# Optimization experiments

Measured on AMD Instinct MI355X. Metric: run time of the kernel, lower is better.

Reference implementation:

```python
import jax, jax.numpy as jnp
import numpy as np

E = 1024
H = 16
DH = E // H
S = 2048
K_NEIGHBOURS = 64
MASKING_VALUE = -1e10  # fp32 branch of the original module


def setup_inputs() -> dict:
    key = jax.random.key(0)
    ks = jax.random.split(key, 5)
    return {
        "x": jax.random.normal(ks[0], (S, E), dtype=jnp.float32),
        "W_qkv": jax.random.normal(ks[1], (3 * E, E), dtype=jnp.float32) * (E ** -0.5),
        "b_qkv": jax.random.normal(ks[2], (3 * E,), dtype=jnp.float32) * 0.02,
        "W_out": jax.random.normal(ks[3], (E, E), dtype=jnp.float32) * (E ** -0.5),
        "b_out": jax.random.normal(ks[4], (E,), dtype=jnp.float32) * 0.02,
    }


def _heads(t):
    # 's (h d) -> h s d'
    return t.reshape(S, H, DH).transpose(1, 0, 2)


def reference(x, W_qkv, b_qkv, W_out, b_out):
    scale = DH ** -0.5
    qkv = x @ W_qkv.T + b_qkv                      # [S, 3E]
    q, k, v = jnp.split(qkv, 3, axis=-1)
    q, k, v = _heads(q), _heads(k), _heads(v)      # [H, S, DH]
    scores = jnp.einsum('hsd,htd->hst', q, k) * scale  # [H, S, S]
    # banded mask: keep |i-j| <= K_NEIGHBOURS
    idx = jnp.arange(S)
    band = jnp.abs(idx[:, None] - idx[None, :]) <= K_NEIGHBOURS  # [S, S]
    scores = jnp.where(band[None, :, :], scores, MASKING_VALUE)
    attn = jax.nn.softmax(scores, axis=-1)
    out = jnp.einsum('hst,htd->hsd', attn, v)      # [H, S, DH]
    out = out.transpose(1, 0, 2).reshape(S, E)      # 'h s d -> s (h d)'
    out = out @ W_out.T + b_out
    return (out, scores)
```

## Files before the change

kernel.cpp:

```cpp
#include <hip/hip_runtime.h>

typedef unsigned short u16;
typedef __attribute__((ext_vector_type(8))) short short8;
typedef __attribute__((ext_vector_type(4))) short short4v;
typedef __attribute__((ext_vector_type(4))) float f32x4;

#define S_LEN 2048
#define EMB   1024
#define NH    16
#define DHD   64
#define NEGM  (-1e10f)

__device__ __forceinline__ u16 f2bf(float f) {
  unsigned u = __float_as_uint(f);
  u += 0x7fffu + ((u >> 16) & 1u);
  return (u16)(u >> 16);
}

__device__ __forceinline__ void async16(const u16* g, u16* l) {
  __builtin_amdgcn_global_load_lds(
      (const __attribute__((address_space(1))) unsigned int*)g,
      (__attribute__((address_space(3))) unsigned int*)l, 16, 0, 0);
}

__global__ __launch_bounds__(256) void cast_bf16_kernel(
    const float* __restrict__ in, u16* __restrict__ out, int n) {
  int t = (blockIdx.x * 256 + threadIdx.x) * 8;
  if (t >= n) return;
  float4 a = *(const float4*)(in + t);
  float4 b = *(const float4*)(in + t + 4);
  u16 r[8];
  r[0] = f2bf(a.x); r[1] = f2bf(a.y); r[2] = f2bf(a.z); r[3] = f2bf(a.w);
  r[4] = f2bf(b.x); r[5] = f2bf(b.y); r[6] = f2bf(b.z); r[7] = f2bf(b.w);
  *(short8*)(out + t) = *(short8*)r;
}

__global__ __launch_bounds__(256, 2) void gemm_bt(
    const u16* __restrict__ A, const u16* __restrict__ B,
    const float* __restrict__ bias, void* __restrict__ Cout,
    int M, int N, int K, int out_bf16) {
  __shared__ u16 As[128 * 64];
  __shared__ u16 Bs[128 * 64];
  const int tid = threadIdx.x;
  const int lane = tid & 63, wave = tid >> 6;
  const int lr = lane & 15, lg = lane >> 4;
  const int m0 = blockIdx.y * 128, n0 = blockIdx.x * 128;
  const int wm = (wave >> 1) * 64, wn = (wave & 1) * 64;

  f32x4 acc[4][4];
#pragma unroll
  for (int i = 0; i < 4; ++i)
#pragma unroll
    for (int j = 0; j < 4; ++j) acc[i][j] = (f32x4){0.f, 0.f, 0.f, 0.f};

  for (int kt = 0; kt < K; kt += 64) {
#pragma unroll
    for (int it = 0; it < 4; ++it) {
      int f = it * 256 + tid;
      int row = f >> 3, ch = f & 7;
      int sch = ch ^ (row & 7);
      const u16* ga = A + (size_t)(m0 + row) * K + kt + sch * 8;
      const u16* gb = B + (size_t)(n0 + row) * K + kt + sch * 8;
      u16* la = &As[(it * 256 + wave * 64) * 8];
      u16* lb = &Bs[(it * 256 + wave * 64) * 8];
      async16(ga, la);
      async16(gb, lb);
    }
    __syncthreads();
#pragma unroll
    for (int kk = 0; kk < 2; ++kk) {
      short8 af[4], bfr[4];
#pragma unroll
      for (int t = 0; t < 4; ++t) {
        int ra = wm + t * 16 + lr;
        int ca = kk * 4 + lg;
        af[t] = *(const short8*)&As[ra * 64 + ((ca ^ (ra & 7)) << 3)];
        int rb = wn + t * 16 + lr;
        bfr[t] = *(const short8*)&Bs[rb * 64 + ((ca ^ (rb & 7)) << 3)];
      }
#pragma unroll
      for (int i = 0; i < 4; ++i)
#pragma unroll
        for (int j = 0; j < 4; ++j)
          acc[i][j] = __builtin_amdgcn_mfma_f32_16x16x32_bf16(af[i], bfr[j],
                                                              acc[i][j], 0, 0, 0);
    }
    __syncthreads();
  }
#pragma unroll
  for (int j = 0; j < 4; ++j) {
    int col = n0 + wn + j * 16 + lr;
    float bv = bias[col];
#pragma unroll
    for (int i = 0; i < 4; ++i) {
#pragma unroll
      for (int r = 0; r < 4; ++r) {
        int row = m0 + wm + i * 16 + lg * 4 + r;
        float v = acc[i][j][r] + bv;
        if (out_bf16)
          ((u16*)Cout)[(size_t)row * N + col] = f2bf(v);
        else
          ((float*)Cout)[(size_t)row * N + col] = v;
      }
    }
  }
}

__global__ __launch_bounds__(256, 2) void attn_kernel(
    const u16* __restrict__ qkv,
    float* __restrict__ scores,
    u16* __restrict__ ctx) {
  const int h = blockIdx.y;
  const int i0 = blockIdx.x * 64;
  const int j0 = i0 - 64;
  const int tid = threadIdx.x;
  const int lane = tid & 63, wave = tid >> 6;
  const int lr = lane & 15, lg = lane >> 4;

  __shared__ u16 Kl[192 * 72];
  __shared__ u16 Vt[64 * 200];
  __shared__ u16 Pl[64 * 200];

#pragma unroll
  for (int it = 0; it < 6; ++it) {
    int f = it * 256 + tid;
    int jr = f >> 3, ch = f & 7;
    int j = j0 + jr;
    short8 kv = {0, 0, 0, 0, 0, 0, 0, 0};
    short8 vv = {0, 0, 0, 0, 0, 0, 0, 0};
    if ((unsigned)j < 2048u) {
      kv = *(const short8*)(qkv + (size_t)j * 3072 + 1024 + h * 64 + ch * 8);
      vv = *(const short8*)(qkv + (size_t)j * 3072 + 2048 + h * 64 + ch * 8);
    }
    *(short4v*)&Kl[jr * 72 + ch * 8] = __builtin_shufflevector(kv, kv, 0, 1, 2, 3);
    *(short4v*)&Kl[jr * 72 + ch * 8 + 4] = __builtin_shufflevector(kv, kv, 4, 5, 6, 7);
#pragma unroll
    for (int e = 0; e < 8; ++e) Vt[(ch * 8 + e) * 200 + jr] = (u16)(short)vv[e];
  }
  __syncthreads();

  short8 qf[2];
#pragma unroll
  for (int kk = 0; kk < 2; ++kk)
    qf[kk] = *(const short8*)(qkv + (size_t)(i0 + wave * 16 + lr) * 3072 +
                              h * 64 + kk * 32 + lg * 8);

  f32x4 sa[12];
#pragma unroll
  for (int n = 0; n < 12; ++n) sa[n] = (f32x4){0.f, 0.f, 0.f, 0.f};
#pragma unroll
  for (int kk = 0; kk < 2; ++kk) {
    short8 a = qf[kk];
#pragma unroll
    for (int nt = 0; nt < 12; ++nt) {
      int jr = nt * 16 + lr;
      int d = kk * 32 + lg * 8;
      short4v lo = *(const short4v*)&Kl[jr * 72 + d];
      short4v hi = *(const short4v*)&Kl[jr * 72 + d + 4];
      short8 b = __builtin_shufflevector(lo, hi, 0, 1, 2, 3, 4, 5, 6, 7);
      sa[nt] = __builtin_amdgcn_mfma_f32_16x16x32_bf16(a, b, sa[nt], 0, 0, 0);
    }
  }

  const float scale = 0.125f;
#pragma unroll
  for (int nt = 0; nt < 12; ++nt) {
    int j = j0 + nt * 16 + lr;
#pragma unroll
    for (int r = 0; r < 4; ++r) {
      int i = i0 + wave * 16 + lg * 4 + r;
      bool inb = (j >= 0) && (j < 2048) && (j >= i - 64) && (j <= i + 64);
      sa[nt][r] = inb ? sa[nt][r] * scale : NEGM;
    }
  }

  float* srow_base = scores + (size_t)h * 2048 * 2048;

#pragma unroll
  for (int r = 0; r < 4; ++r) {
    int i = i0 + wave * 16 + lg * 4 + r;
    float* rowp = srow_base + (size_t)i * 2048;
#pragma unroll
    for (int nt = 0; nt < 12; ++nt) {
      int j = j0 + nt * 16 + lr;
      if (j >= 0 && j < 2048 && j >= i - 64 && j <= i + 64) rowp[j] = sa[nt][r];
    }
  }

#pragma unroll
  for (int r = 0; r < 4; ++r) {
    float m = sa[0][r];
#pragma unroll
    for (int nt = 1; nt < 12; ++nt) m = fmaxf(m, sa[nt][r]);
#pragma unroll
    for (int off = 1; off < 16; off <<= 1) m = fmaxf(m, __shfl_xor(m, off));
    float p[12], s = 0.f;
#pragma unroll
    for (int nt = 0; nt < 12; ++nt) {
      p[nt] = __expf(sa[nt][r] - m);
      s += p[nt];
    }
#pragma unroll
    for (int off = 1; off < 16; off <<= 1) s += __shfl_xor(s, off);
    float inv = 1.f / s;
    int row = wave * 16 + lg * 4 + r;
#pragma unroll
    for (int nt = 0; nt < 12; ++nt)
      Pl[row * 200 + nt * 16 + lr] = f2bf(p[nt] * inv);
  }
  __syncthreads();

  f32x4 ca[4];
#pragma unroll
  for (int d = 0; d < 4; ++d) ca[d] = (f32x4){0.f, 0.f, 0.f, 0.f};
#pragma unroll
  for (int kk = 0; kk < 6; ++kk) {
    short8 a = *(const short8*)&Pl[(wave * 16 + lr) * 200 + kk * 32 + lg * 8];
#pragma unroll
    for (int dt = 0; dt < 4; ++dt) {
      short8 b = *(const short8*)&Vt[(dt * 16 + lr) * 200 + kk * 32 + lg * 8];
      ca[dt] = __builtin_amdgcn_mfma_f32_16x16x32_bf16(a, b, ca[dt], 0, 0, 0);
    }
  }
#pragma unroll
  for (int dt = 0; dt < 4; ++dt)
#pragma unroll
    for (int r = 0; r < 4; ++r) {
      int i = i0 + wave * 16 + lg * 4 + r;
      int d = h * 64 + dt * 16 + lr;
      ctx[(size_t)i * 1024 + d] = f2bf(ca[dt][r]);
    }

  float4 negv = {NEGM, NEGM, NEGM, NEGM};
  for (int r = 0; r < 64; ++r) {
    int i = i0 + r;
    int li = (i - 64 > 0) ? (i - 64) : 0;
    int ri = ((i + 64 < 2047) ? (i + 64) : 2047) + 1;
    float* rowp = srow_base + (size_t)i * 2048;
    for (int c = tid; c < 512; c += 256) {
      int j4 = c << 2;
      if (j4 + 4 <= li || j4 >= ri) {
        *(float4*)(rowp + j4) = negv;
      } else if (j4 < li || j4 + 4 > ri) {
#pragma unroll
        for (int e = 0; e < 4; ++e) {
          int jj = j4 + e;
          if (jj < li || jj >= ri) rowp[jj] = NEGM;
        }
      }
    }
  }
}

extern "C" void kernel_launch(void* const* d_in, const int* in_sizes, int n_in,
                              void* d_out, int out_size, void* d_ws, size_t ws_size,
                              hipStream_t stream) {
  const float* x    = (const float*)d_in[0];
  const float* Wqkv = (const float*)d_in[1];
  const float* bqkv = (const float*)d_in[2];
  const float* Wout = (const float*)d_in[3];
  const float* bout = (const float*)d_in[4];

  float* out    = (float*)d_out;
  float* scores = out + (size_t)S_LEN * EMB;

  char* ws = (char*)d_ws;
  u16* x_bf    = (u16*)(ws);
  u16* wqkv_bf = (u16*)(ws + (4u << 20));
  u16* wout_bf = (u16*)(ws + (10u << 20));
  u16* qkv_bf  = (u16*)(ws + (12u << 20));
  u16* ctx_bf  = (u16*)(ws + (24u << 20));

  const int n1 = S_LEN * EMB;
  const int n2 = 3 * EMB * EMB;
  const int n3 = EMB * EMB;
  cast_bf16_kernel<<<n1 / 8 / 256, 256, 0, stream>>>(x, x_bf, n1);
  cast_bf16_kernel<<<n2 / 8 / 256, 256, 0, stream>>>(Wqkv, wqkv_bf, n2);
  cast_bf16_kernel<<<n3 / 8 / 256, 256, 0, stream>>>(Wout, wout_bf, n3);

  gemm_bt<<<dim3(3 * EMB / 128, S_LEN / 128), 256, 0, stream>>>(
      x_bf, wqkv_bf, bqkv, qkv_bf, S_LEN, 3 * EMB, EMB, 1);

  attn_kernel<<<dim3(S_LEN / 64, NH), 256, 0, stream>>>(qkv_bf, scores, ctx_bf);

  gemm_bt<<<dim3(EMB / 128, S_LEN / 128), 256, 0, stream>>>(
      ctx_bf, wout_bf, bout, out, S_LEN, EMB, EMB, 0);
}
```

Baseline: 381.1 us.

## Overlap masked-score fill with QKV GEMM and merge the cast launches

The full -1e10 fill of the scores tensor moves out of the attention kernel into extra blocks of the QKV GEMM launch, using nontemporal stores so the bandwidth-bound fill runs alongside compute-bound GEMM work. The attention kernel then writes its whole 192-wide window (masked values included) with nontemporal stores, overwriting the prefilled values. The three cast kernels are merged into one launch. The output projection switches to 64x128 tiles to give 256 blocks instead of 128. This relies on the fill finishing before attention writes, which stream ordering guarantees. The fill blocks compete with GEMM blocks for CUs.

```diff
diff --git a/kernel.cpp b/kernel.cpp
--- a/kernel.cpp
+++ b/kernel.cpp
@@ -8,7 +8,6 @@
 #define S_LEN 2048
 #define EMB   1024
 #define NH    16
-#define DHD   64
 #define NEGM  (-1e10f)
 
 __device__ __forceinline__ u16 f2bf(float f) {
@@ -23,81 +22,111 @@
       (__attribute__((address_space(3))) unsigned int*)l, 16, 0, 0);
 }
 
-__global__ __launch_bounds__(256) void cast_bf16_kernel(
-    const float* __restrict__ in, u16* __restrict__ out, int n) {
+__global__ __launch_bounds__(256) void cast3_kernel(
+    const float* __restrict__ a, u16* __restrict__ oa, int na,
+    const float* __restrict__ b, u16* __restrict__ ob, int nb,
+    const float* __restrict__ c, u16* __restrict__ oc, int nc) {
   int t = (blockIdx.x * 256 + threadIdx.x) * 8;
-  if (t >= n) return;
-  float4 a = *(const float4*)(in + t);
-  float4 b = *(const float4*)(in + t + 4);
+  const float* in;
+  u16* out;
+  if (t < na) { in = a + t; out = oa + t; }
+  else if (t < na + nb) { in = b + (t - na); out = ob + (t - na); }
+  else if (t < na + nb + nc) { in = c + (t - na - nb); out = oc + (t - na - nb); }
+  else return;
+  f32x4 lo = *(const f32x4*)(in);
+  f32x4 hi = *(const f32x4*)(in + 4);
   u16 r[8];
-  r[0] = f2bf(a.x); r[1] = f2bf(a.y); r[2] = f2bf(a.z); r[3] = f2bf(a.w);
-  r[4] = f2bf(b.x); r[5] = f2bf(b.y); r[6] = f2bf(b.z); r[7] = f2bf(b.w);
-  *(short8*)(out + t) = *(short8*)r;
-}
-
-__global__ __launch_bounds__(256, 2) void gemm_bt(
+  r[0] = f2bf(lo.x); r[1] = f2bf(lo.y); r[2] = f2bf(lo.z); r[3] = f2bf(lo.w);
+  r[4] = f2bf(hi.x); r[5] = f2bf(hi.y); r[6] = f2bf(hi.z); r[7] = f2bf(hi.w);
+  *(short8*)(out) = *(short8*)r;
+}
+
+template <int BM, int BN, int OUT_BF16, int MINW>
+__global__ __launch_bounds__(256, MINW) void gemm_kernel(
     const u16* __restrict__ A, const u16* __restrict__ B,
     const float* __restrict__ bias, void* __restrict__ Cout,
-    int M, int N, int K, int out_bf16) {
-  __shared__ u16 As[128 * 64];
-  __shared__ u16 Bs[128 * 64];
+    int M, int N, int K, int grid_x, int gemm_blocks,
+    float* __restrict__ fill_ptr, long long fill_f4, int fill_blocks) {
+  __shared__ u16 As[BM * 64];
+  __shared__ u16 Bs[BN * 64];
+  const int b = blockIdx.x;
   const int tid = threadIdx.x;
+
+  if (b >= gemm_blocks) {
+    const long long fb = b - gemm_blocks;
+    f32x4 neg = {NEGM, NEGM, NEGM, NEGM};
+    f32x4* p = (f32x4*)fill_ptr;
+    const long long stride = (long long)fill_blocks * 256;
+    for (long long idx = fb * 256 + tid; idx < fill_f4; idx += stride)
+      __builtin_nontemporal_store(neg, p + idx);
+    return;
+  }
+
   const int lane = tid & 63, wave = tid >> 6;
   const int lr = lane & 15, lg = lane >> 4;
-  const int m0 = blockIdx.y * 128, n0 = blockIdx.x * 128;
-  const int wm = (wave >> 1) * 64, wn = (wave & 1) * 64;
-
-  f32x4 acc[4][4];
-#pragma unroll
-  for (int i = 0; i < 4; ++i)
-#pragma unroll
-    for (int j = 0; j < 4; ++j) acc[i][j] = (f32x4){0.f, 0.f, 0.f, 0.f};
+  const int bx = b % grid_x, by = b / grid_x;
+  const int m0 = by * BM, n0 = bx * BN;
+  const int wm = (wave >> 1) * (BM / 2), wn = (wave & 1) * (BN / 2);
+  constexpr int MI = BM / 32, NJ = BN / 32;
+
+  f32x4 acc[MI][NJ];
+#pragma unroll
+  for (int i = 0; i < MI; ++i)
+#pragma unroll
+    for (int j = 0; j < NJ; ++j) acc[i][j] = (f32x4){0.f, 0.f, 0.f, 0.f};
 
   for (int kt = 0; kt < K; kt += 64) {
 #pragma unroll
-    for (int it = 0; it < 4; ++it) {
+    for (int it = 0; it < BM / 32; ++it) {
       int f = it * 256 + tid;
       int row = f >> 3, ch = f & 7;
       int sch = ch ^ (row & 7);
-      const u16* ga = A + (size_t)(m0 + row) * K + kt + sch * 8;
-      const u16* gb = B + (size_t)(n0 + row) * K + kt + sch * 8;
-      u16* la = &As[(it * 256 + wave * 64) * 8];
-      u16* lb = &Bs[(it * 256 + wave * 64) * 8];
-      async16(ga, la);
-      async16(gb, lb);
+      async16(A + (size_t)(m0 + row) * K + kt + sch * 8,
+              &As[(it * 256 + wave * 64) * 8]);
+    }
+#pragma unroll
+    for (int it = 0; it < BN / 32; ++it) {
+      int f = it * 256 + tid;
+      int row = f >> 3, ch = f & 7;
+      int sch = ch ^ (row & 7);
+      async16(B + (size_t)(n0 + row) * K + kt + sch * 8,
+              &Bs[(it * 256 + wave * 64) * 8]);
     }
     __syncthreads();
 #pragma unroll
     for (int kk = 0; kk < 2; ++kk) {
-      short8 af[4], bfr[4];
-#pragma unroll
-      for (int t = 0; t < 4; ++t) {
+      short8 af[MI], bfr[NJ];
+      int ca = kk * 4 + lg;
+#pragma unroll
+      for (int t = 0; t < MI; ++t) {
         int ra = wm + t * 16 + lr;
-        int ca = kk * 4 + lg;
         af[t] = *(const short8*)&As[ra * 64 + ((ca ^ (ra & 7)) << 3)];
+      }
+#pragma unroll
+      for (int t = 0; t < NJ; ++t) {
         int rb = wn + t * 16 + lr;
         bfr[t] = *(const short8*)&Bs[rb * 64 + ((ca ^ (rb & 7)) << 3)];
       }
 #pragma unroll
-      for (int i = 0; i < 4; ++i)
-#pragma unroll
-        for (int j = 0; j < 4; ++j)
+      for (int i = 0; i < MI; ++i)
+#pragma unroll
+        for (int j = 0; j < NJ; ++j)
           acc[i][j] = __builtin_amdgcn_mfma_f32_16x16x32_bf16(af[i], bfr[j],
                                                               acc[i][j], 0, 0, 0);
     }
     __syncthreads();
   }
 #pragma unroll
-  for (int j = 0; j < 4; ++j) {
+  for (int j = 0; j < NJ; ++j) {
     int col = n0 + wn + j * 16 + lr;
     float bv = bias[col];
 #pragma unroll
-    for (int i = 0; i < 4; ++i) {
+    for (int i = 0; i < MI; ++i) {
 #pragma unroll
       for (int r = 0; r < 4; ++r) {
         int row = m0 + wm + i * 16 + lg * 4 + r;
         float v = acc[i][j][r] + bv;
-        if (out_bf16)
+        if (OUT_BF16)
           ((u16*)Cout)[(size_t)row * N + col] = f2bf(v);
         else
           ((float*)Cout)[(size_t)row * N + col] = v;
@@ -169,13 +198,12 @@
 #pragma unroll
     for (int r = 0; r < 4; ++r) {
       int i = i0 + wave * 16 + lg * 4 + r;
-      bool inb = (j >= 0) && (j < 2048) && (j >= i - 64) && (j <= i + 64);
+      bool inb = (j >= i - 64) && (j <= i + 64);
       sa[nt][r] = inb ? sa[nt][r] * scale : NEGM;
     }
   }
 
   float* srow_base = scores + (size_t)h * 2048 * 2048;
-
 #pragma unroll
   for (int r = 0; r < 4; ++r) {
     int i = i0 + wave * 16 + lg * 4 + r;
@@ -183,7 +211,7 @@
 #pragma unroll
     for (int nt = 0; nt < 12; ++nt) {
       int j = j0 + nt * 16 + lr;
-      if (j >= 0 && j < 2048 && j >= i - 64 && j <= i + 64) rowp[j] = sa[nt][r];
+      if ((unsigned)j < 2048u) __builtin_nontemporal_store(sa[nt][r], rowp + j);
     }
   }
 
@@ -230,26 +258,6 @@
       int d = h * 64 + dt * 16 + lr;
       ctx[(size_t)i * 1024 + d] = f2bf(ca[dt][r]);
     }
-
-  float4 negv = {NEGM, NEGM, NEGM, NEGM};
-  for (int r = 0; r < 64; ++r) {
-    int i = i0 + r;
-    int li = (i - 64 > 0) ? (i - 64) : 0;
-    int ri = ((i + 64 < 2047) ? (i + 64) : 2047) + 1;
-    float* rowp = srow_base + (size_t)i * 2048;
-    for (int c = tid; c < 512; c += 256) {
-      int j4 = c << 2;
-      if (j4 + 4 <= li || j4 >= ri) {
-        *(float4*)(rowp + j4) = negv;
-      } else if (j4 < li || j4 + 4 > ri) {
-#pragma unroll
-        for (int e = 0; e < 4; ++e) {
-          int jj = j4 + e;
-          if (jj < li || jj >= ri) rowp[jj] = NEGM;
-        }
-      }
-    }
-  }
 }
 
 extern "C" void kernel_launch(void* const* d_in, const int* in_sizes, int n_in,
@@ -274,15 +282,20 @@
   const int n1 = S_LEN * EMB;
   const int n2 = 3 * EMB * EMB;
   const int n3 = EMB * EMB;
-  cast_bf16_kernel<<<n1 / 8 / 256, 256, 0, stream>>>(x, x_bf, n1);
-  cast_bf16_kernel<<<n2 / 8 / 256, 256, 0, stream>>>(Wqkv, wqkv_bf, n2);
-  cast_bf16_kernel<<<n3 / 8 / 256, 256, 0, stream>>>(Wout, wout_bf, n3);
-
-  gemm_bt<<<dim3(3 * EMB / 128, S_LEN / 128), 256, 0, stream>>>(
-      x_bf, wqkv_bf, bqkv, qkv_bf, S_LEN, 3 * EMB, EMB, 1);
+
+  cast3_kernel<<<(n1 + n2 + n3) / 8 / 256, 256, 0, stream>>>(
+      x, x_bf, n1, Wqkv, wqkv_bf, n2, Wout, wout_bf, n3);
+
+  const long long fill_f4 = (long long)NH * S_LEN * S_LEN / 4;
+  gemm_kernel<128, 128, 1, 3><<<768, 256, 0, stream>>>(
+      x_bf, wqkv_bf, bqkv, qkv_bf, S_LEN, 3 * EMB, EMB,
+      3 * EMB / 128, 384,
+      scores, fill_f4, 384);
 
   attn_kernel<<<dim3(S_LEN / 64, NH), 256, 0, stream>>>(qkv_bf, scores, ctx_bf);
 
-  gemm_bt<<<dim3(EMB / 128, S_LEN / 128), 256, 0, stream>>>(
-      ctx_bf, wout_bf, bout, out, S_LEN, EMB, EMB, 0);
-}
+  gemm_kernel<64, 128, 0, 2><<<256, 256, 0, stream>>>(
+      ctx_bf, wout_bf, bout, out, S_LEN, EMB, EMB,
+      EMB / 128, 256,
+      nullptr, 0, 0);
+}
```

Result: faster. 332.7 us (-12.7%).
